# Optimization experiments

Hardware: AMD Instinct MI355X
Metric: run time of the kernel (lower is better)

The kernel has to match this reference:

```python
import jax, jax.numpy as jnp
import numpy as np

B, P, ENC = 64, 196, 2048
A = H = E = 512
V = 30000
L = 30  # max caption length; T = L-1 decode steps


def setup_inputs() -> dict:
    key = jax.random.key(0)
    ks = jax.random.split(key, 24)
    s = 0.02
    lengths = jax.random.randint(ks[1], (B, 1), 2, L + 1)
    lengths = lengths.at[0, 0].set(L)  # ensure max length present
    return {
        "encoder_out": jax.random.normal(ks[0], (B, P, ENC), dtype=jnp.float32),
        "enc_att_w": jax.random.normal(ks[2], (A, ENC), jnp.float32) * s,
        "enc_att_b": jnp.zeros((A,), jnp.float32),
        "dec_att_w": jax.random.normal(ks[3], (A, H), jnp.float32) * s,
        "dec_att_b": jnp.zeros((A,), jnp.float32),
        "full_att_w": jax.random.normal(ks[4], (1, A), jnp.float32) * s,
        "full_att_b": jnp.zeros((1,), jnp.float32),
        "embed": jax.random.uniform(ks[5], (V, E), jnp.float32, -0.1, 0.1),
        "W_ih": jax.random.normal(ks[6], (4 * H, E + ENC), jnp.float32) * s,
        "W_hh": jax.random.normal(ks[7], (4 * H, H), jnp.float32) * s,
        "b_ih": jnp.zeros((4 * H,), jnp.float32),
        "b_hh": jnp.zeros((4 * H,), jnp.float32),
        "init_h_w": jax.random.normal(ks[8], (H, ENC), jnp.float32) * s,
        "init_h_b": jnp.zeros((H,), jnp.float32),
        "init_c_w": jax.random.normal(ks[9], (H, ENC), jnp.float32) * s,
        "init_c_b": jnp.zeros((H,), jnp.float32),
        "f_beta_w": jax.random.normal(ks[10], (ENC, H), jnp.float32) * s,
        "f_beta_b": jnp.zeros((ENC,), jnp.float32),
        "fc_w": jax.random.uniform(ks[11], (V, H), jnp.float32, -0.1, 0.1),
        "fc_b": jnp.zeros((V,), jnp.float32),
        "encoded_captions": jax.random.randint(ks[12], (B, L), 0, V),
        "caption_lengths": lengths,
    }


def reference(encoder_out, enc_att_w, enc_att_b, dec_att_w, dec_att_b, full_att_w,
              full_att_b, embed, W_ih, W_hh, b_ih, b_hh, init_h_w, init_h_b,
              init_c_w, init_c_b, f_beta_w, f_beta_b, fc_w, fc_b,
              encoded_captions, caption_lengths):
    # sort by caption length descending (as in the torch module)
    lengths = caption_lengths[:, 0]
    sort_ind = jnp.argsort(-lengths)
    lengths = lengths[sort_ind]
    enc = encoder_out[sort_ind]               # [B,P,ENC]
    caps = encoded_captions[sort_ind]         # [B,L]
    embeds = embed[caps]                      # [B,L,E]

    mean_enc = enc.mean(axis=1)
    h0 = mean_enc @ init_h_w.T + init_h_b     # [B,H]
    c0 = mean_enc @ init_c_w.T + init_c_b
    dec_len = lengths - 1
    T = caps.shape[1] - 1

    att1 = enc @ enc_att_w.T + enc_att_b      # [B,P,A] (precompute, invariant over t)

    def step(carry, emb_t):
        h, c = carry
        att2 = h @ dec_att_w.T + dec_att_b                                    # [B,A]
        e = jnp.squeeze(jax.nn.relu(att1 + att2[:, None, :]) @ full_att_w.T + full_att_b, -1)  # [B,P]
        alpha = jax.nn.softmax(e, axis=1)
        awe = jnp.einsum('bp,bpd->bd', alpha, enc)                            # [B,ENC]
        gate = jax.nn.sigmoid(h @ f_beta_w.T + f_beta_b)
        awe = gate * awe
        x = jnp.concatenate([emb_t, awe], axis=1)                             # [B,E+ENC]
        gates = x @ W_ih.T + b_ih + h @ W_hh.T + b_hh                         # [B,4H]
        i, f, g, o = jnp.split(gates, 4, axis=1)
        c_new = jax.nn.sigmoid(f) * c + jax.nn.sigmoid(i) * jnp.tanh(g)
        h_new = jax.nn.sigmoid(o) * jnp.tanh(c_new)
        preds = h_new @ fc_w.T + fc_b  # dropout in eval mode = identity
        return (h_new, c_new), (preds, alpha)

    _, (preds, alphas) = jax.lax.scan(step, (h0, c0), jnp.swapaxes(embeds[:, :T], 0, 1))
    preds = jnp.swapaxes(preds, 0, 1)   # [B,T,V]
    alphas = jnp.swapaxes(alphas, 0, 1)  # [B,T,P]
    mask = (jnp.arange(T)[None, :] < dec_len[:, None]).astype(preds.dtype)
    preds = preds * mask[:, :, None]
    alphas = alphas * mask[:, :, None]
    return preds, caps, dec_len, alphas, sort_ind
```

## Files before the change

### kernel.cpp

```cpp
#include <hip/hip_runtime.h>
#include <hip/hip_bf16.h>
#include <cstdint>

#define Bq 64
#define Pq 196
#define ENCq 2048
#define Aq 512
#define Hq 512
#define Vq 30000
#define Lq 30
#define Tq 29

typedef __bf16 bf16x8 __attribute__((ext_vector_type(8)));
typedef float f32x4 __attribute__((ext_vector_type(4)));
typedef __hip_bfloat16 bf16_t;

__device__ __forceinline__ float sigmoidf_(float x){ return 1.0f/(1.0f+expf(-x)); }

__global__ void sort_kernel(const int* __restrict__ cap_len, const int* __restrict__ caps,
                            int* __restrict__ sort_ind_i, int* __restrict__ dec_len_i,
                            int* __restrict__ caps_sorted,
                            float* __restrict__ out_caps, float* __restrict__ out_declen,
                            float* __restrict__ out_sortind)
{
    __shared__ int len[Bq];
    __shared__ int sidx[Bq];
    int i = threadIdx.x;
    len[i] = cap_len[i];
    __syncthreads();
    int li = len[i];
    int rank = 0;
    for (int j = 0; j < Bq; j++){
        int lj = len[j];
        rank += (lj > li) || (lj == li && j < i);
    }
    sidx[rank] = i;
    __syncthreads();
    int src = sidx[i];
    sort_ind_i[i] = src;
    int dl = len[src] - 1;
    dec_len_i[i] = dl;
    out_declen[i] = (float)dl;
    out_sortind[i] = (float)src;
    for (int tt = 0; tt < Lq; tt++){
        int cv = caps[src*Lq + tt];
        caps_sorted[i*Lq + tt] = cv;
        out_caps[i*Lq + tt] = (float)cv;
    }
}

__global__ void cvt_bf16(bf16_t* __restrict__ dst, const float* __restrict__ src, int n)
{
    int i = blockIdx.x*256 + threadIdx.x;
    if (i < n) dst[i] = __float2bfloat16(src[i]);
}

__global__ void pack_rowcat_bf16(bf16_t* __restrict__ dst, const float* __restrict__ a, int na,
                                 const float* __restrict__ b, int nb)
{
    int i = blockIdx.x*256 + threadIdx.x;
    if (i < na) dst[i] = __float2bfloat16(a[i]);
    else if (i < na + nb) dst[i] = __float2bfloat16(b[i - na]);
}

__global__ void pack_rowcat_f32(float* __restrict__ dst, const float* __restrict__ a, int na,
                                const float* __restrict__ b, int nb)
{
    int i = blockIdx.x*256 + threadIdx.x;
    if (i < na) dst[i] = a[i];
    else if (i < na + nb) dst[i] = b[i - na];
}

__global__ void pack_wcatg2(bf16_t* __restrict__ dst, const float* __restrict__ wih,
                            const float* __restrict__ whh)
{
    int i = blockIdx.x*256 + threadIdx.x;
    if (i >= 2048*2560) return;
    int rp = i / 2560, c = i % 2560;
    int g = rp & 3, j = rp >> 2;
    int r = g*512 + j;
    float v = (c < 2048) ? wih[(size_t)r*2560 + 512 + c] : whh[(size_t)r*512 + (c - 2048)];
    dst[i] = __float2bfloat16(v);
}

__global__ void pack_wembg(bf16_t* __restrict__ dst, const float* __restrict__ wih)
{
    int i = blockIdx.x*256 + threadIdx.x;
    if (i >= 2048*512) return;
    int rp = i >> 9, c = i & 511;
    int g = rp & 3, j = rp >> 2;
    int r = g*512 + j;
    dst[i] = __float2bfloat16(wih[(size_t)r*2560 + c]);
}

__global__ void biasg_perm_kernel(float* __restrict__ dst, const float* __restrict__ bi,
                                  const float* __restrict__ bh)
{
    int i = blockIdx.x*256 + threadIdx.x;
    if (i >= 2048) return;
    int g = i & 3, j = i >> 2;
    int r = g*512 + j;
    dst[i] = bi[r] + bh[r];
}

__global__ void gather_emb(const float* __restrict__ embed, const int* __restrict__ caps_sorted,
                           bf16_t* __restrict__ embA)
{
    int m = blockIdx.x;
    int t = m >> 6, b = m & 63;
    int cap = caps_sorted[b*Lq + t];
    const float* er = embed + (size_t)cap*512;
    bf16_t* dr = embA + (size_t)m*512;
    for (int j = threadIdx.x; j < 512; j += 256) dr[j] = __float2bfloat16(er[j]);
}

__global__ __launch_bounds__(256)
void gather_cvt_mean(const float* __restrict__ enc, const int* __restrict__ sort_ind,
                     bf16_t* __restrict__ enc_bf, bf16_t* __restrict__ mean_bf)
{
    int b = blockIdx.x;
    int d = blockIdx.y*256 + threadIdx.x;
    int src = sort_ind[b];
    const float* col = enc + (size_t)src * Pq * ENCq + d;
    bf16_t* dst = enc_bf + (size_t)b * Pq * ENCq + d;
    float s = 0.f;
    for (int p = 0; p < Pq; p++){
        float v = col[(size_t)p*ENCq];
        s += v;
        dst[(size_t)p*ENCq] = __float2bfloat16(v);
    }
    mean_bf[(size_t)b*ENCq + d] = __float2bfloat16(s * (1.0f/196.0f));
}

__global__ __launch_bounds__(256)
void hc0_ksplit(const bf16_t* __restrict__ A, const bf16_t* __restrict__ W,
                const float* __restrict__ bias,
                bf16_t* __restrict__ h0, float* __restrict__ c_state)
{
    __shared__ float red[2][64][64];
    const int lane = threadIdx.x & 63;
    const int wave = threadIdx.x >> 6;
    const int mr = lane & 15;
    const int quad = lane >> 4;
    const int n0 = blockIdx.x * 64;
    const int kw = 2048 >> 2;
    const int kbeg = wave * kw;

    const bf16_t* ap[4];
    const bf16_t* bp[4];
    #pragma unroll
    for (int i = 0; i < 4; i++){
        ap[i] = A + (size_t)(i*16 + mr)*2048 + quad*8;
        bp[i] = W + (size_t)(n0 + i*16 + mr)*2048 + quad*8;
    }
    f32x4 zero = {0.f,0.f,0.f,0.f};
    f32x4 acc[4][4];
    #pragma unroll
    for (int i = 0; i < 4; i++)
        #pragma unroll
        for (int j = 0; j < 4; j++) acc[i][j] = zero;

    for (int k = kbeg; k < kbeg + kw; k += 32){
        bf16x8 a[4], b[4];
        #pragma unroll
        for (int mt = 0; mt < 4; mt++) a[mt] = *(const bf16x8*)(ap[mt] + k);
        #pragma unroll
        for (int nt = 0; nt < 4; nt++) b[nt] = *(const bf16x8*)(bp[nt] + k);
        #pragma unroll
        for (int mt = 0; mt < 4; mt++)
            #pragma unroll
            for (int nt = 0; nt < 4; nt++)
                acc[mt][nt] = __builtin_amdgcn_mfma_f32_16x16x32_bf16(a[mt], b[nt], acc[mt][nt], 0, 0, 0);
    }

    if (wave >= 2){
        #pragma unroll
        for (int mt = 0; mt < 4; mt++)
            #pragma unroll
            for (int nt = 0; nt < 4; nt++)
                #pragma unroll
                for (int r = 0; r < 4; r++)
                    red[wave-2][mt*16 + quad*4 + r][nt*16 + mr] = acc[mt][nt][r];
    }
    __syncthreads();
    if (wave < 2){
        #pragma unroll
        for (int mt = 0; mt < 4; mt++)
            #pragma unroll
            for (int nt = 0; nt < 4; nt++)
                #pragma unroll
                for (int r = 0; r < 4; r++)
                    acc[mt][nt][r] += red[wave][mt*16 + quad*4 + r][nt*16 + mr];
    }
    __syncthreads();
    if (wave == 1){
        #pragma unroll
        for (int mt = 0; mt < 4; mt++)
            #pragma unroll
            for (int nt = 0; nt < 4; nt++)
                #pragma unroll
                for (int r = 0; r < 4; r++)
                    red[0][mt*16 + quad*4 + r][nt*16 + mr] = acc[mt][nt][r];
    }
    __syncthreads();
    if (wave == 0){
        #pragma unroll
        for (int mt = 0; mt < 4; mt++){
            #pragma unroll
            for (int nt = 0; nt < 4; nt++){
                int n = n0 + nt*16 + mr;
                float bv = bias[n];
                #pragma unroll
                for (int r = 0; r < 4; r++){
                    int m = mt*16 + quad*4 + r;
                    float v = acc[mt][nt][r] + red[0][m][nt*16 + mr] + bv;
                    if (n < Hq) h0[(size_t)m*Hq + n] = __float2bfloat16(v);
                    else        c_state[(size_t)m*Hq + (n - Hq)] = v;
                }
            }
        }
    }
}

__global__ __launch_bounds__(256)
void att1_gemm(const bf16_t* __restrict__ A, const bf16_t* __restrict__ W,
               const float* __restrict__ bias, bf16_t* __restrict__ C)
{
    const int lane = threadIdx.x & 63;
    const int wave = threadIdx.x >> 6;
    const int mr = lane & 15;
    const int quad = lane >> 4;
    const int m0 = blockIdx.x * 64;
    const int n0 = (blockIdx.y * 4 + wave) * 64;

    const bf16_t* ap[4];
    const bf16_t* bp[4];
    #pragma unroll
    for (int i = 0; i < 4; i++){
        ap[i] = A + (size_t)(m0 + i*16 + mr)*ENCq + quad*8;
        bp[i] = W + (size_t)(n0 + i*16 + mr)*ENCq + quad*8;
    }
    f32x4 zero = {0.f,0.f,0.f,0.f};
    f32x4 acc[4][4];
    #pragma unroll
    for (int i = 0; i < 4; i++)
        #pragma unroll
        for (int j = 0; j < 4; j++) acc[i][j] = zero;

    for (int k = 0; k < ENCq; k += 32){
        bf16x8 a[4], b[4];
        #pragma unroll
        for (int mt = 0; mt < 4; mt++) a[mt] = *(const bf16x8*)(ap[mt] + k);
        #pragma unroll
        for (int nt = 0; nt < 4; nt++) b[nt] = *(const bf16x8*)(bp[nt] + k);
        #pragma unroll
        for (int mt = 0; mt < 4; mt++)
            #pragma unroll
            for (int nt = 0; nt < 4; nt++)
                acc[mt][nt] = __builtin_amdgcn_mfma_f32_16x16x32_bf16(a[mt], b[nt], acc[mt][nt], 0, 0, 0);
    }
    #pragma unroll
    for (int mt = 0; mt < 4; mt++){
        #pragma unroll
        for (int nt = 0; nt < 4; nt++){
            int n = n0 + nt*16 + mr;
            float bv = bias[n];
            #pragma unroll
            for (int r = 0; r < 4; r++){
                int m = m0 + mt*16 + quad*4 + r;
                C[(size_t)m*Aq + n] = __float2bfloat16(acc[mt][nt][r] + bv);
            }
        }
    }
}

__global__ __launch_bounds__(256)
void embg_gemm(const bf16_t* __restrict__ A, const bf16_t* __restrict__ W,
               float* __restrict__ C)
{
    const int lane = threadIdx.x & 63;
    const int wave = threadIdx.x >> 6;
    const int mr = lane & 15;
    const int quad = lane >> 4;
    const int m0 = blockIdx.x * 64;
    const int n0 = (blockIdx.y * 4 + wave) * 64;

    const bf16_t* ap[4];
    const bf16_t* bp[4];
    #pragma unroll
    for (int i = 0; i < 4; i++){
        ap[i] = A + (size_t)(m0 + i*16 + mr)*512 + quad*8;
        bp[i] = W + (size_t)(n0 + i*16 + mr)*512 + quad*8;
    }
    f32x4 zero = {0.f,0.f,0.f,0.f};
    f32x4 acc[4][4];
    #pragma unroll
    for (int i = 0; i < 4; i++)
        #pragma unroll
        for (int j = 0; j < 4; j++) acc[i][j] = zero;

    #pragma unroll
    for (int kk = 0; kk < 16; kk++){
        bf16x8 a[4], b[4];
        #pragma unroll
        for (int mt = 0; mt < 4; mt++) a[mt] = *(const bf16x8*)(ap[mt] + kk*32);
        #pragma unroll
        for (int nt = 0; nt < 4; nt++) b[nt] = *(const bf16x8*)(bp[nt] + kk*32);
        #pragma unroll
        for (int mt = 0; mt < 4; mt++)
            #pragma unroll
            for (int nt = 0; nt < 4; nt++)
                acc[mt][nt] = __builtin_amdgcn_mfma_f32_16x16x32_bf16(a[mt], b[nt], acc[mt][nt], 0, 0, 0);
    }
    #pragma unroll
    for (int mt = 0; mt < 4; mt++){
        #pragma unroll
        for (int nt = 0; nt < 4; nt++){
            int n = n0 + nt*16 + mr;
            #pragma unroll
            for (int r = 0; r < 4; r++){
                int m = m0 + mt*16 + quad*4 + r;
                C[(size_t)m*2048 + n] = acc[mt][nt][r];
            }
        }
    }
}

__global__ __launch_bounds__(256)
void attg_gemm(const bf16_t* __restrict__ h, const bf16_t* __restrict__ W,
               const float* __restrict__ bias, float* __restrict__ C)
{
    __shared__ __bf16 hs[64][520];
    {
        int r = threadIdx.x >> 2;
        int c0 = (threadIdx.x & 3) * 128;
        const bf16_t* src = h + (size_t)r*512 + c0;
        #pragma unroll
        for (int i = 0; i < 16; i++)
            *(bf16x8*)&hs[r][c0 + i*8] = *(const bf16x8*)(src + i*8);
    }
    __syncthreads();

    const int lane = threadIdx.x & 63;
    const int wave = threadIdx.x >> 6;
    const int mr = lane & 15;
    const int quad = lane >> 4;
    const int n0 = (blockIdx.x * 4 + wave) * 16;

    const bf16_t* bp = W + (size_t)(n0 + mr)*512 + quad*8;
    f32x4 zero = {0.f,0.f,0.f,0.f};
    f32x4 acc[4] = {zero, zero, zero, zero};

    #pragma unroll
    for (int kk = 0; kk < 16; kk++){
        bf16x8 b = *(const bf16x8*)(bp + kk*32);
        bf16x8 a[4];
        #pragma unroll
        for (int mt = 0; mt < 4; mt++)
            a[mt] = *(const bf16x8*)&hs[mt*16 + mr][kk*32 + quad*8];
        #pragma unroll
        for (int mt = 0; mt < 4; mt++)
            acc[mt] = __builtin_amdgcn_mfma_f32_16x16x32_bf16(a[mt], b, acc[mt], 0, 0, 0);
    }

    float bv = bias[n0 + mr];
    #pragma unroll
    for (int mt = 0; mt < 4; mt++){
        #pragma unroll
        for (int r = 0; r < 4; r++){
            int m = mt*16 + quad*4 + r;
            C[(size_t)m*2560 + n0 + mr] = acc[mt][r] + bv;
        }
    }
}

__global__ __launch_bounds__(256)
void gates_lstm2(const bf16_t* __restrict__ A, const bf16_t* __restrict__ W,
                 const float* __restrict__ bias, const float* __restrict__ gE,
                 float* __restrict__ c_state, bf16_t* __restrict__ h_next)
{
    __shared__ float red4[2][64][17];
    const int lane = threadIdx.x & 63;
    const int wid  = threadIdx.x >> 6;
    const int mr = lane & 15;
    const int quad = lane >> 4;
    const int n0 = blockIdx.x * 16;
    const int kbeg = wid * 640;

    const bf16_t* ap[4];
    #pragma unroll
    for (int i = 0; i < 4; i++) ap[i] = A + (size_t)(i*16 + mr)*2560 + quad*8;
    const bf16_t* bp = W + (size_t)(n0 + mr)*2560 + quad*8;

    f32x4 zero = {0.f,0.f,0.f,0.f};
    f32x4 acc[4] = {zero, zero, zero, zero};
    for (int k = kbeg; k < kbeg + 640; k += 32){
        bf16x8 bfr = *(const bf16x8*)(bp + k);
        bf16x8 a[4];
        #pragma unroll
        for (int mt = 0; mt < 4; mt++) a[mt] = *(const bf16x8*)(ap[mt] + k);
        #pragma unroll
        for (int mt = 0; mt < 4; mt++)
            acc[mt] = __builtin_amdgcn_mfma_f32_16x16x32_bf16(a[mt], bfr, acc[mt], 0, 0, 0);
    }
    if (wid >= 2){
        #pragma unroll
        for (int mt = 0; mt < 4; mt++)
            #pragma unroll
            for (int r = 0; r < 4; r++)
                red4[wid-2][mt*16 + quad*4 + r][mr] = acc[mt][r];
    }
    __syncthreads();
    if (wid < 2){
        #pragma unroll
        for (int mt = 0; mt < 4; mt++)
            #pragma unroll
            for (int r = 0; r < 4; r++)
                acc[mt][r] += red4[wid][mt*16 + quad*4 + r][mr];
    }
    __syncthreads();
    if (wid == 1){
        #pragma unroll
        for (int mt = 0; mt < 4; mt++)
            #pragma unroll
            for (int r = 0; r < 4; r++)
                red4[0][mt*16 + quad*4 + r][mr] = acc[mt][r];
    }
    __syncthreads();
    if (wid == 0){
        float bv = bias[n0 + mr];
        #pragma unroll
        for (int mt = 0; mt < 4; mt++){
            #pragma unroll
            for (int r = 0; r < 4; r++){
                int m = mt*16 + quad*4 + r;
                float ge = gE[(size_t)m*2048 + n0 + mr];
                red4[0][m][mr] = acc[mt][r] + red4[0][m][mr] + bv + ge;
            }
        }
    }
    __syncthreads();
    {
        int m = threadIdx.x & 63, jl = threadIdx.x >> 6;
        int j = blockIdx.x*4 + jl;
        float gi = sigmoidf_(red4[0][m][4*jl + 0]);
        float gf = sigmoidf_(red4[0][m][4*jl + 1]);
        float gv = tanhf(red4[0][m][4*jl + 2]);
        float go = sigmoidf_(red4[0][m][4*jl + 3]);
        float cc = c_state[m*512 + j];
        float cn = gf*cc + gi*gv;
        float hn = go * tanhf(cn);
        c_state[m*512 + j] = cn;
        h_next[m*512 + j] = __float2bfloat16(hn);
    }
}

__global__ __launch_bounds__(256)
void preds_batched(const bf16_t* __restrict__ Ah, const bf16_t* __restrict__ W,
                   const float* __restrict__ bias, float* __restrict__ C,
                   const int* __restrict__ dec_len)
{
    const int lane = threadIdx.x & 63;
    const int wave = threadIdx.x >> 6;
    const int mr = lane & 15;
    const int quad = lane >> 4;
    const int m0 = blockIdx.x * 256 + wave * 64;
    const int n0 = blockIdx.y * 64;

    const bf16_t* ap[4];
    const bf16_t* bp[4];
    #pragma unroll
    for (int i = 0; i < 4; i++){
        int row = m0 + i*16 + mr; if (row > 1855) row = 1855;
        ap[i] = Ah + (size_t)row*512 + quad*8;
        int n = n0 + i*16 + mr;   if (n > Vq-1) n = Vq-1;
        bp[i] = W + (size_t)n*512 + quad*8;
    }
    f32x4 zero = {0.f,0.f,0.f,0.f};
    f32x4 acc[4][4];
    #pragma unroll
    for (int i = 0; i < 4; i++)
        #pragma unroll
        for (int j = 0; j < 4; j++) acc[i][j] = zero;

    #pragma unroll
    for (int kk = 0; kk < 16; kk++){
        bf16x8 a[4], b[4];
        #pragma unroll
        for (int mt = 0; mt < 4; mt++) a[mt] = *(const bf16x8*)(ap[mt] + kk*32);
        #pragma unroll
        for (int nt = 0; nt < 4; nt++) b[nt] = *(const bf16x8*)(bp[nt] + kk*32);
        #pragma unroll
        for (int mt = 0; mt < 4; mt++)
            #pragma unroll
            for (int nt = 0; nt < 4; nt++)
                acc[mt][nt] = __builtin_amdgcn_mfma_f32_16x16x32_bf16(b[nt], a[mt], acc[mt][nt], 0, 0, 0);
    }

    #pragma unroll
    for (int mt = 0; mt < 4; mt++){
        int m = m0 + mt*16 + mr;
        if (m >= 1856) continue;
        int tt = m >> 6, b = m & 63;
        bool msk = (tt >= dec_len[b]);
        float* crow = C + (size_t)b*(Tq*Vq) + (size_t)tt*Vq;
        #pragma unroll
        for (int nt = 0; nt < 4; nt++){
            int n = n0 + nt*16 + quad*4;
            if (n < Vq){
                float4 bv = *(const float4*)(bias + n);
                f32x4 v = acc[mt][nt];
                float4 o;
                o.x = msk ? 0.f : (v[0] + bv.x);
                o.y = msk ? 0.f : (v[1] + bv.y);
                o.z = msk ? 0.f : (v[2] + bv.z);
                o.w = msk ? 0.f : (v[3] + bv.w);
                *(float4*)(crow + n) = o;
            }
        }
    }
}

__global__ __launch_bounds__(256)
void attn_kernel(const bf16_t* __restrict__ att1,
                 const float* __restrict__ att2gate,
                 const float* __restrict__ faw, const float* __restrict__ fab,
                 const int* __restrict__ dec_len,
                 float* __restrict__ alpha_ws,
                 float* __restrict__ alphas_out, int t)
{
    __shared__ float es[Pq];
    __shared__ float red[8];
    int b = blockIdx.x;
    int tid = threadIdx.x;
    int wid = tid >> 6, lane = tid & 63;

    float a2r[8], fwr[8];
    {
        const float4* a2p = (const float4*)(att2gate + (size_t)b*2560);
        const float4* fwp = (const float4*)faw;
        float4 u0 = a2p[lane*2], u1 = a2p[lane*2+1];
        float4 w0 = fwp[lane*2], w1 = fwp[lane*2+1];
        a2r[0]=u0.x; a2r[1]=u0.y; a2r[2]=u0.z; a2r[3]=u0.w;
        a2r[4]=u1.x; a2r[5]=u1.y; a2r[6]=u1.z; a2r[7]=u1.w;
        fwr[0]=w0.x; fwr[1]=w0.y; fwr[2]=w0.z; fwr[3]=w0.w;
        fwr[4]=w1.x; fwr[5]=w1.y; fwr[6]=w1.z; fwr[7]=w1.w;
    }
    float fb = fab[0];
    const bf16_t* a1b = att1 + (size_t)b * Pq * Aq + lane*8;
    for (int p = wid; p < Pq; p += 4){
        bf16x8 rv = *(const bf16x8*)(a1b + (size_t)p * Aq);
        float s = 0.f;
        #pragma unroll
        for (int i = 0; i < 8; i++){
            float v = (float)rv[i] + a2r[i];
            v = v > 0.f ? v : 0.f;
            s += v * fwr[i];
        }
        #pragma unroll
        for (int off = 32; off; off >>= 1) s += __shfl_xor(s, off);
        if (lane == 0) es[p] = s + fb;
    }
    __syncthreads();
    float v = (tid < Pq) ? es[tid] : -3.4e38f;
    float m = v;
    #pragma unroll
    for (int off = 32; off; off >>= 1) m = fmaxf(m, __shfl_xor(m, off));
    if ((tid & 63) == 0) red[tid >> 6] = m;
    __syncthreads();
    float bm = fmaxf(fmaxf(red[0], red[1]), fmaxf(red[2], red[3]));
    float ex = (tid < Pq) ? expf(v - bm) : 0.f;
    float s = ex;
    #pragma unroll
    for (int off = 32; off; off >>= 1) s += __shfl_xor(s, off);
    if ((tid & 63) == 0) red[4 + (tid >> 6)] = s;
    __syncthreads();
    float bs = red[4] + red[5] + red[6] + red[7];
    if (tid < Pq){
        float al = ex / bs;
        alpha_ws[b*Pq + tid] = al;
        float mask = (t < dec_len[b]) ? 1.f : 0.f;
        alphas_out[((size_t)b*Tq + t)*Pq + tid] = al * mask;
    }
}

__global__ __launch_bounds__(256)
void awe_xcat2(const bf16_t* __restrict__ enc_bf,
               const float* __restrict__ att2gate,
               const float* __restrict__ alpha_ws,
               const bf16_t* __restrict__ h_prev,
               bf16_t* __restrict__ xcat2)
{
    int b = blockIdx.x, y = blockIdx.y, tid = threadIdx.x;
    __shared__ float als[Pq];
    if (tid < Pq) als[tid] = alpha_ws[b*Pq + tid];
    __syncthreads();
    int d = y*256 + tid;
    const bf16_t* ebase = enc_bf + (size_t)b * Pq * ENCq + d;
    float s = 0.f;
    #pragma unroll 4
    for (int p = 0; p < Pq; p++) s += als[p] * (float)ebase[(size_t)p*ENCq];
    float g = sigmoidf_(att2gate[(size_t)b*2560 + 512 + d]);
    xcat2[(size_t)b*2560 + d] = __float2bfloat16(g * s);
    if (y == 0){
        for (int j = tid; j < 512; j += 256)
            xcat2[(size_t)b*2560 + 2048 + j] = h_prev[b*512 + j];
    }
}

extern "C" void kernel_launch(void* const* d_in, const int* in_sizes, int n_in,
                              void* d_out, int out_size, void* d_ws, size_t ws_size,
                              hipStream_t stream)
{
    const float* encoder_out = (const float*)d_in[0];
    const float* enc_att_w   = (const float*)d_in[1];
    const float* enc_att_b   = (const float*)d_in[2];
    const float* dec_att_w   = (const float*)d_in[3];
    const float* dec_att_b   = (const float*)d_in[4];
    const float* full_att_w  = (const float*)d_in[5];
    const float* full_att_b  = (const float*)d_in[6];
    const float* embed       = (const float*)d_in[7];
    const float* W_ih        = (const float*)d_in[8];
    const float* W_hh        = (const float*)d_in[9];
    const float* b_ih        = (const float*)d_in[10];
    const float* b_hh        = (const float*)d_in[11];
    const float* init_h_w    = (const float*)d_in[12];
    const float* init_h_b    = (const float*)d_in[13];
    const float* init_c_w    = (const float*)d_in[14];
    const float* init_c_b    = (const float*)d_in[15];
    const float* f_beta_w    = (const float*)d_in[16];
    const float* f_beta_b    = (const float*)d_in[17];
    const float* fc_w        = (const float*)d_in[18];
    const float* fc_b        = (const float*)d_in[19];
    const int*   enc_caps    = (const int*)d_in[20];
    const int*   cap_len     = (const int*)d_in[21];

    float* out_preds   = (float*)d_out;
    float* out_caps    = out_preds + (size_t)Bq*Tq*Vq;
    float* out_declen  = out_caps + Bq*Lq;
    float* out_alphas  = out_declen + Bq;
    float* out_sortind = out_alphas + (size_t)Bq*Tq*Pq;

    char* cur = (char*)d_ws;
    auto alloc = [&](size_t bytes) -> char* {
        char* p = cur;
        cur += (bytes + 255) & ~(size_t)255;
        return p;
    };
    bf16_t* enc_bf    = (bf16_t*)alloc((size_t)12544*2048*2);
    bf16_t* att1_bf   = (bf16_t*)alloc((size_t)12544*512*2);
    bf16_t* fcw_bf    = (bf16_t*)alloc((size_t)30000*512*2);
    bf16_t* wcatg_bf  = (bf16_t*)alloc((size_t)2048*2560*2);
    bf16_t* wembg_bf  = (bf16_t*)alloc((size_t)2048*512*2);
    bf16_t* embA_bf   = (bf16_t*)alloc((size_t)1856*512*2);
    float*  gatesE    = (float*)alloc((size_t)1856*2048*4);
    bf16_t* whc_bf    = (bf16_t*)alloc((size_t)1024*2048*2);
    bf16_t* wcat2_bf  = (bf16_t*)alloc((size_t)2560*512*2);
    bf16_t* encattw_bf= (bf16_t*)alloc((size_t)512*2048*2);
    bf16_t* meanenc_bf= (bf16_t*)alloc((size_t)64*2048*2);
    bf16_t* h_hist    = (bf16_t*)alloc((size_t)30*64*512*2);
    bf16_t* xcat2_bf  = (bf16_t*)alloc((size_t)64*2560*2);
    float* c_state   = (float*)alloc((size_t)64*512*4);
    float* att2gate  = (float*)alloc((size_t)64*2560*4);
    float* bias_hc   = (float*)alloc(1024*4);
    float* bias2     = (float*)alloc(2560*4);
    float* bias_g    = (float*)alloc(2048*4);
    float* alpha_ws  = (float*)alloc((size_t)64*196*4);
    int* caps_sorted = (int*)alloc(Bq*Lq*4);
    int* sort_ind_i  = (int*)alloc(64*4);
    int* dec_len_i   = (int*)alloc(64*4);

    sort_kernel<<<1, 64, 0, stream>>>(cap_len, enc_caps, sort_ind_i, dec_len_i,
                                      caps_sorted, out_caps, out_declen, out_sortind);

    cvt_bf16<<<(1048576+255)/256, 256, 0, stream>>>(encattw_bf, enc_att_w, 1048576);
    cvt_bf16<<<(15360000+255)/256, 256, 0, stream>>>(fcw_bf, fc_w, 15360000);
    pack_rowcat_bf16<<<(2097152+255)/256, 256, 0, stream>>>(whc_bf, init_h_w, 1048576, init_c_w, 1048576);
    pack_rowcat_bf16<<<(1310720+255)/256, 256, 0, stream>>>(wcat2_bf, dec_att_w, 262144, f_beta_w, 1048576);
    pack_wcatg2<<<(2048*2560+255)/256, 256, 0, stream>>>(wcatg_bf, W_ih, W_hh);
    pack_wembg<<<(2048*512+255)/256, 256, 0, stream>>>(wembg_bf, W_ih);
    pack_rowcat_f32<<<(1024+255)/256, 256, 0, stream>>>(bias_hc, init_h_b, 512, init_c_b, 512);
    pack_rowcat_f32<<<(2560+255)/256, 256, 0, stream>>>(bias2, dec_att_b, 512, f_beta_b, 2048);
    biasg_perm_kernel<<<8, 256, 0, stream>>>(bias_g, b_ih, b_hh);

    gather_emb<<<1856, 256, 0, stream>>>(embed, caps_sorted, embA_bf);
    embg_gemm<<<dim3(29,8), 256, 0, stream>>>(embA_bf, wembg_bf, gatesE);

    gather_cvt_mean<<<dim3(64,8), 256, 0, stream>>>(encoder_out, sort_ind_i, enc_bf, meanenc_bf);

    hc0_ksplit<<<16, 256, 0, stream>>>(meanenc_bf, whc_bf, bias_hc, h_hist, c_state);

    att1_gemm<<<dim3(196,2), 256, 0, stream>>>(enc_bf, encattw_bf, enc_att_b, att1_bf);

    for (int t = 0; t < Tq; t++){
        const bf16_t* h_prev = h_hist + (size_t)t*Bq*Hq;
        bf16_t* h_next = h_hist + (size_t)(t+1)*Bq*Hq;

        attg_gemm<<<40, 256, 0, stream>>>(h_prev, wcat2_bf, bias2, att2gate);

        attn_kernel<<<64, 256, 0, stream>>>(att1_bf, att2gate, full_att_w, full_att_b,
                                            dec_len_i, alpha_ws, out_alphas, t);

        awe_xcat2<<<dim3(64,8), 256, 0, stream>>>(enc_bf, att2gate, alpha_ws, h_prev, xcat2_bf);

        gates_lstm2<<<128, 256, 0, stream>>>(xcat2_bf, wcatg_bf, bias_g,
                                             gatesE + (size_t)t*64*2048, c_state, h_next);
    }

    preds_batched<<<dim3(8,469), 256, 0, stream>>>(h_hist + (size_t)Bq*Hq, fcw_bf, fc_b,
                                                   out_preds, dec_len_i);
}
```

Before: 3.005 ms.

## Fuse per-step attention projections, softmax and gated context into one kernel

```diff
diff --git a/kernel.cpp b/kernel.cpp
--- a/kernel.cpp
+++ b/kernel.cpp
@@ -12,6 +12,7 @@
 #define Tq 29
 
 typedef __bf16 bf16x8 __attribute__((ext_vector_type(8)));
+typedef __bf16 bf16x4 __attribute__((ext_vector_type(4)));
 typedef float f32x4 __attribute__((ext_vector_type(4)));
 typedef __hip_bfloat16 bf16_t;
 
@@ -326,52 +327,130 @@
     }
 }
 
-__global__ __launch_bounds__(256)
-void attg_gemm(const bf16_t* __restrict__ h, const bf16_t* __restrict__ W,
-               const float* __restrict__ bias, float* __restrict__ C)
-{
-    __shared__ __bf16 hs[64][520];
+__global__ __launch_bounds__(512)
+void attn_fused(const bf16_t* __restrict__ att1, const bf16_t* __restrict__ wcat2,
+                const float* __restrict__ bias2, const float* __restrict__ faw,
+                const float* __restrict__ fab, const int* __restrict__ dec_len,
+                const bf16_t* __restrict__ enc_bf, const bf16_t* __restrict__ h_prev,
+                float* __restrict__ alphas_out, bf16_t* __restrict__ xcat2, int t)
+{
+    __shared__ float hls[512];
+    __shared__ float a2s[512];
+    __shared__ float es[Pq];
+    __shared__ float als[Pq];
+    __shared__ float red[16];
+    const int b = blockIdx.x;
+    const int tid = threadIdx.x;
+    const int wid = tid >> 6, lane = tid & 63;
+    const bf16_t* hp = h_prev + (size_t)b*512;
+
+    if (tid < 64){
+        bf16x8 hv = ((const bf16x8*)hp)[tid];
+        #pragma unroll
+        for (int i = 0; i < 8; i++) hls[tid*8 + i] = (float)hv[i];
+    }
+    __syncthreads();
+
     {
-        int r = threadIdx.x >> 2;
-        int c0 = (threadIdx.x & 3) * 128;
-        const bf16_t* src = h + (size_t)r*512 + c0;
-        #pragma unroll
-        for (int i = 0; i < 16; i++)
-            *(bf16x8*)&hs[r][c0 + i*8] = *(const bf16x8*)(src + i*8);
-    }
-    __syncthreads();
-
-    const int lane = threadIdx.x & 63;
-    const int wave = threadIdx.x >> 6;
-    const int mr = lane & 15;
-    const int quad = lane >> 4;
-    const int n0 = (blockIdx.x * 4 + wave) * 16;
-
-    const bf16_t* bp = W + (size_t)(n0 + mr)*512 + quad*8;
-    f32x4 zero = {0.f,0.f,0.f,0.f};
-    f32x4 acc[4] = {zero, zero, zero, zero};
-
-    #pragma unroll
-    for (int kk = 0; kk < 16; kk++){
-        bf16x8 b = *(const bf16x8*)(bp + kk*32);
-        bf16x8 a[4];
-        #pragma unroll
-        for (int mt = 0; mt < 4; mt++)
-            a[mt] = *(const bf16x8*)&hs[mt*16 + mr][kk*32 + quad*8];
-        #pragma unroll
-        for (int mt = 0; mt < 4; mt++)
-            acc[mt] = __builtin_amdgcn_mfma_f32_16x16x32_bf16(a[mt], b, acc[mt], 0, 0, 0);
-    }
-
-    float bv = bias[n0 + mr];
-    #pragma unroll
-    for (int mt = 0; mt < 4; mt++){
+        const bf16_t* wr = wcat2 + (size_t)tid*512;
+        float s = 0.f;
+        for (int k = 0; k < 512; k += 8){
+            bf16x8 w = *(const bf16x8*)(wr + k);
+            float4 h0 = *(const float4*)&hls[k];
+            float4 h1 = *(const float4*)&hls[k+4];
+            s += h0.x*(float)w[0] + h0.y*(float)w[1] + h0.z*(float)w[2] + h0.w*(float)w[3]
+               + h1.x*(float)w[4] + h1.y*(float)w[5] + h1.z*(float)w[6] + h1.w*(float)w[7];
+        }
+        a2s[tid] = s + bias2[tid];
+    }
+    __syncthreads();
+
+    {
+        float a2r[8], fwr[8];
+        const float4* fwp = (const float4*)faw;
+        float4 w0 = fwp[lane*2], w1 = fwp[lane*2+1];
+        fwr[0]=w0.x; fwr[1]=w0.y; fwr[2]=w0.z; fwr[3]=w0.w;
+        fwr[4]=w1.x; fwr[5]=w1.y; fwr[6]=w1.z; fwr[7]=w1.w;
+        #pragma unroll
+        for (int i = 0; i < 8; i++) a2r[i] = a2s[lane*8 + i];
+        float fb = fab[0];
+        const bf16_t* a1b = att1 + (size_t)b * Pq * Aq + lane*8;
+        for (int p = wid; p < Pq; p += 8){
+            bf16x8 rv = *(const bf16x8*)(a1b + (size_t)p * Aq);
+            float s = 0.f;
+            #pragma unroll
+            for (int i = 0; i < 8; i++){
+                float v = (float)rv[i] + a2r[i];
+                v = v > 0.f ? v : 0.f;
+                s += v * fwr[i];
+            }
+            #pragma unroll
+            for (int off = 32; off; off >>= 1) s += __shfl_xor(s, off);
+            if (lane == 0) es[p] = s + fb;
+        }
+    }
+    __syncthreads();
+
+    {
+        float v = (tid < Pq) ? es[tid] : -3.4e38f;
+        float m = v;
+        #pragma unroll
+        for (int off = 32; off; off >>= 1) m = fmaxf(m, __shfl_xor(m, off));
+        if (lane == 0) red[wid] = m;
+        __syncthreads();
+        float bm = red[0];
+        #pragma unroll
+        for (int w = 1; w < 8; w++) bm = fmaxf(bm, red[w]);
+        float ex = (tid < Pq) ? expf(v - bm) : 0.f;
+        float s = ex;
+        #pragma unroll
+        for (int off = 32; off; off >>= 1) s += __shfl_xor(s, off);
+        if (lane == 0) red[8 + wid] = s;
+        __syncthreads();
+        float bs = red[8];
+        #pragma unroll
+        for (int w = 1; w < 8; w++) bs += red[8 + w];
+        if (tid < Pq){
+            float al = ex / bs;
+            als[tid] = al;
+            float mask = (t < dec_len[b]) ? 1.f : 0.f;
+            alphas_out[((size_t)b*Tq + t)*Pq + tid] = al * mask;
+        }
+    }
+    __syncthreads();
+
+    {
+        const int d0 = tid * 4;
+        const bf16_t* wr = wcat2 + (size_t)(512 + d0)*512;
+        f32x4 gs = {0.f,0.f,0.f,0.f};
+        for (int k = 0; k < 512; k += 8){
+            float4 h0 = *(const float4*)&hls[k];
+            float4 h1 = *(const float4*)&hls[k+4];
+            #pragma unroll
+            for (int r = 0; r < 4; r++){
+                bf16x8 w = *(const bf16x8*)(wr + (size_t)r*512 + k);
+                gs[r] += h0.x*(float)w[0] + h0.y*(float)w[1] + h0.z*(float)w[2] + h0.w*(float)w[3]
+                       + h1.x*(float)w[4] + h1.y*(float)w[5] + h1.z*(float)w[6] + h1.w*(float)w[7];
+            }
+        }
+        const bf16_t* eb = enc_bf + (size_t)b * Pq * ENCq + d0;
+        f32x4 sa = {0.f,0.f,0.f,0.f};
+        for (int p = 0; p < Pq; p++){
+            bf16x4 ev = *(const bf16x4*)(eb + (size_t)p*ENCq);
+            float al = als[p];
+            sa[0] += al*(float)ev[0];
+            sa[1] += al*(float)ev[1];
+            sa[2] += al*(float)ev[2];
+            sa[3] += al*(float)ev[3];
+        }
+        bf16_t* xo = xcat2 + (size_t)b*2560 + d0;
         #pragma unroll
         for (int r = 0; r < 4; r++){
-            int m = mt*16 + quad*4 + r;
-            C[(size_t)m*2560 + n0 + mr] = acc[mt][r] + bv;
-        }
-    }
+            float g = sigmoidf_(gs[r] + bias2[512 + d0 + r]);
+            xo[r] = __float2bfloat16(g * sa[r]);
+        }
+    }
+    xcat2[(size_t)b*2560 + 2048 + tid] = hp[tid];
 }
 
 __global__ __launch_bounds__(256)
@@ -456,155 +535,78 @@
 }
 
 __global__ __launch_bounds__(256)
-void preds_batched(const bf16_t* __restrict__ Ah, const bf16_t* __restrict__ W,
-                   const float* __restrict__ bias, float* __restrict__ C,
-                   const int* __restrict__ dec_len)
-{
-    const int lane = threadIdx.x & 63;
-    const int wave = threadIdx.x >> 6;
+void preds_batched2(const bf16_t* __restrict__ Ah, const bf16_t* __restrict__ W,
+                    const float* __restrict__ bias, float* __restrict__ C,
+                    const int* __restrict__ dec_len)
+{
+    __shared__ __bf16 Ws[64][520];
+    const int tid = threadIdx.x;
+    const int lane = tid & 63;
+    const int wave = tid >> 6;
     const int mr = lane & 15;
     const int quad = lane >> 4;
-    const int m0 = blockIdx.x * 256 + wave * 64;
-    const int n0 = blockIdx.y * 64;
-
-    const bf16_t* ap[4];
-    const bf16_t* bp[4];
-    #pragma unroll
-    for (int i = 0; i < 4; i++){
-        int row = m0 + i*16 + mr; if (row > 1855) row = 1855;
-        ap[i] = Ah + (size_t)row*512 + quad*8;
-        int n = n0 + i*16 + mr;   if (n > Vq-1) n = Vq-1;
-        bp[i] = W + (size_t)n*512 + quad*8;
-    }
-    f32x4 zero = {0.f,0.f,0.f,0.f};
-    f32x4 acc[4][4];
-    #pragma unroll
-    for (int i = 0; i < 4; i++)
-        #pragma unroll
-        for (int j = 0; j < 4; j++) acc[i][j] = zero;
-
-    #pragma unroll
-    for (int kk = 0; kk < 16; kk++){
-        bf16x8 a[4], b[4];
-        #pragma unroll
-        for (int mt = 0; mt < 4; mt++) a[mt] = *(const bf16x8*)(ap[mt] + kk*32);
-        #pragma unroll
-        for (int nt = 0; nt < 4; nt++) b[nt] = *(const bf16x8*)(bp[nt] + kk*32);
-        #pragma unroll
-        for (int mt = 0; mt < 4; mt++)
-            #pragma unroll
-            for (int nt = 0; nt < 4; nt++)
-                acc[mt][nt] = __builtin_amdgcn_mfma_f32_16x16x32_bf16(b[nt], a[mt], acc[mt][nt], 0, 0, 0);
-    }
-
-    #pragma unroll
-    for (int mt = 0; mt < 4; mt++){
-        int m = m0 + mt*16 + mr;
-        if (m >= 1856) continue;
-        int tt = m >> 6, b = m & 63;
-        bool msk = (tt >= dec_len[b]);
-        float* crow = C + (size_t)b*(Tq*Vq) + (size_t)tt*Vq;
-        #pragma unroll
-        for (int nt = 0; nt < 4; nt++){
-            int n = n0 + nt*16 + quad*4;
-            if (n < Vq){
-                float4 bv = *(const float4*)(bias + n);
-                f32x4 v = acc[mt][nt];
-                float4 o;
-                o.x = msk ? 0.f : (v[0] + bv.x);
-                o.y = msk ? 0.f : (v[1] + bv.y);
-                o.z = msk ? 0.f : (v[2] + bv.z);
-                o.w = msk ? 0.f : (v[3] + bv.w);
-                *(float4*)(crow + n) = o;
+    const int n0 = blockIdx.x * 64;
+
+    {
+        int r = tid >> 2;
+        int c0 = (tid & 3) * 128;
+        int row = n0 + r; if (row > Vq-1) row = Vq-1;
+        const bf16_t* src = W + (size_t)row*512 + c0;
+        #pragma unroll
+        for (int i = 0; i < 16; i++)
+            *(bf16x8*)&Ws[r][c0 + i*8] = *(const bf16x8*)(src + i*8);
+    }
+    __syncthreads();
+
+    for (int mi = wave; mi < 29; mi += 4){
+        const int m0 = mi * 64;
+        const bf16_t* ap[4];
+        #pragma unroll
+        for (int i = 0; i < 4; i++)
+            ap[i] = Ah + (size_t)(m0 + i*16 + mr)*512 + quad*8;
+
+        f32x4 zero = {0.f,0.f,0.f,0.f};
+        f32x4 acc[4][4];
+        #pragma unroll
+        for (int i = 0; i < 4; i++)
+            #pragma unroll
+            for (int j = 0; j < 4; j++) acc[i][j] = zero;
+
+        #pragma unroll
+        for (int kk = 0; kk < 16; kk++){
+            bf16x8 a[4], bw[4];
+            #pragma unroll
+            for (int mt = 0; mt < 4; mt++) a[mt] = *(const bf16x8*)(ap[mt] + kk*32);
+            #pragma unroll
+            for (int nt = 0; nt < 4; nt++) bw[nt] = *(const bf16x8*)&Ws[nt*16 + mr][kk*32 + quad*8];
+            #pragma unroll
+            for (int mt = 0; mt < 4; mt++)
+                #pragma unroll
+                for (int nt = 0; nt < 4; nt++)
+                    acc[mt][nt] = __builtin_amdgcn_mfma_f32_16x16x32_bf16(bw[nt], a[mt], acc[mt][nt], 0, 0, 0);
+        }
+
+        #pragma unroll
+        for (int mt = 0; mt < 4; mt++){
+            int m = m0 + mt*16 + mr;
+            int tt = m >> 6, bb = m & 63;
+            bool msk = (tt >= dec_len[bb]);
+            float* crow = C + (size_t)bb*(Tq*Vq) + (size_t)tt*Vq;
+            #pragma unroll
+            for (int nt = 0; nt < 4; nt++){
+                int n = n0 + nt*16 + quad*4;
+                if (n < Vq){
+                    float4 bv = *(const float4*)(bias + n);
+                    f32x4 v = acc[mt][nt];
+                    float4 o;
+                    o.x = msk ? 0.f : (v[0] + bv.x);
+                    o.y = msk ? 0.f : (v[1] + bv.y);
+                    o.z = msk ? 0.f : (v[2] + bv.z);
+                    o.w = msk ? 0.f : (v[3] + bv.w);
+                    *(float4*)(crow + n) = o;
+                }
             }
         }
-    }
-}
-
-__global__ __launch_bounds__(256)
-void attn_kernel(const bf16_t* __restrict__ att1,
-                 const float* __restrict__ att2gate,
-                 const float* __restrict__ faw, const float* __restrict__ fab,
-                 const int* __restrict__ dec_len,
-                 float* __restrict__ alpha_ws,
-                 float* __restrict__ alphas_out, int t)
-{
-    __shared__ float es[Pq];
-    __shared__ float red[8];
-    int b = blockIdx.x;
-    int tid = threadIdx.x;
-    int wid = tid >> 6, lane = tid & 63;
-
-    float a2r[8], fwr[8];
-    {
-        const float4* a2p = (const float4*)(att2gate + (size_t)b*2560);
-        const float4* fwp = (const float4*)faw;
-        float4 u0 = a2p[lane*2], u1 = a2p[lane*2+1];
-        float4 w0 = fwp[lane*2], w1 = fwp[lane*2+1];
-        a2r[0]=u0.x; a2r[1]=u0.y; a2r[2]=u0.z; a2r[3]=u0.w;
-        a2r[4]=u1.x; a2r[5]=u1.y; a2r[6]=u1.z; a2r[7]=u1.w;
-        fwr[0]=w0.x; fwr[1]=w0.y; fwr[2]=w0.z; fwr[3]=w0.w;
-        fwr[4]=w1.x; fwr[5]=w1.y; fwr[6]=w1.z; fwr[7]=w1.w;
-    }
-    float fb = fab[0];
-    const bf16_t* a1b = att1 + (size_t)b * Pq * Aq + lane*8;
-    for (int p = wid; p < Pq; p += 4){
-        bf16x8 rv = *(const bf16x8*)(a1b + (size_t)p * Aq);
-        float s = 0.f;
-        #pragma unroll
-        for (int i = 0; i < 8; i++){
-            float v = (float)rv[i] + a2r[i];
-            v = v > 0.f ? v : 0.f;
-            s += v * fwr[i];
-        }
-        #pragma unroll
-        for (int off = 32; off; off >>= 1) s += __shfl_xor(s, off);
-        if (lane == 0) es[p] = s + fb;
-    }
-    __syncthreads();
-    float v = (tid < Pq) ? es[tid] : -3.4e38f;
-    float m = v;
-    #pragma unroll
-    for (int off = 32; off; off >>= 1) m = fmaxf(m, __shfl_xor(m, off));
-    if ((tid & 63) == 0) red[tid >> 6] = m;
-    __syncthreads();
-    float bm = fmaxf(fmaxf(red[0], red[1]), fmaxf(red[2], red[3]));
-    float ex = (tid < Pq) ? expf(v - bm) : 0.f;
-    float s = ex;
-    #pragma unroll
-    for (int off = 32; off; off >>= 1) s += __shfl_xor(s, off);
-    if ((tid & 63) == 0) red[4 + (tid >> 6)] = s;
-    __syncthreads();
-    float bs = red[4] + red[5] + red[6] + red[7];
-    if (tid < Pq){
-        float al = ex / bs;
-        alpha_ws[b*Pq + tid] = al;
-        float mask = (t < dec_len[b]) ? 1.f : 0.f;
-        alphas_out[((size_t)b*Tq + t)*Pq + tid] = al * mask;
-    }
-}
-
-__global__ __launch_bounds__(256)
-void awe_xcat2(const bf16_t* __restrict__ enc_bf,
-               const float* __restrict__ att2gate,
-               const float* __restrict__ alpha_ws,
-               const bf16_t* __restrict__ h_prev,
-               bf16_t* __restrict__ xcat2)
-{
-    int b = blockIdx.x, y = blockIdx.y, tid = threadIdx.x;
-    __shared__ float als[Pq];
-    if (tid < Pq) als[tid] = alpha_ws[b*Pq + tid];
-    __syncthreads();
-    int d = y*256 + tid;
-    const bf16_t* ebase = enc_bf + (size_t)b * Pq * ENCq + d;
-    float s = 0.f;
-    #pragma unroll 4
-    for (int p = 0; p < Pq; p++) s += als[p] * (float)ebase[(size_t)p*ENCq];
-    float g = sigmoidf_(att2gate[(size_t)b*2560 + 512 + d]);
-    xcat2[(size_t)b*2560 + d] = __float2bfloat16(g * s);
-    if (y == 0){
-        for (int j = tid; j < 512; j += 256)
-            xcat2[(size_t)b*2560 + 2048 + j] = h_prev[b*512 + j];
     }
 }
 
@@ -661,11 +663,9 @@
     bf16_t* h_hist    = (bf16_t*)alloc((size_t)30*64*512*2);
     bf16_t* xcat2_bf  = (bf16_t*)alloc((size_t)64*2560*2);
     float* c_state   = (float*)alloc((size_t)64*512*4);
-    float* att2gate  = (float*)alloc((size_t)64*2560*4);
     float* bias_hc   = (float*)alloc(1024*4);
     float* bias2     = (float*)alloc(2560*4);
     float* bias_g    = (float*)alloc(2048*4);
-    float* alpha_ws  = (float*)alloc((size_t)64*196*4);
     int* caps_sorted = (int*)alloc(Bq*Lq*4);
     int* sort_ind_i  = (int*)alloc(64*4);
     int* dec_len_i   = (int*)alloc(64*4);
@@ -696,17 +696,13 @@
         const bf16_t* h_prev = h_hist + (size_t)t*Bq*Hq;
         bf16_t* h_next = h_hist + (size_t)(t+1)*Bq*Hq;
 
-        attg_gemm<<<40, 256, 0, stream>>>(h_prev, wcat2_bf, bias2, att2gate);
-
-        attn_kernel<<<64, 256, 0, stream>>>(att1_bf, att2gate, full_att_w, full_att_b,
-                                            dec_len_i, alpha_ws, out_alphas, t);
-
-        awe_xcat2<<<dim3(64,8), 256, 0, stream>>>(enc_bf, att2gate, alpha_ws, h_prev, xcat2_bf);
+        attn_fused<<<64, 512, 0, stream>>>(att1_bf, wcat2_bf, bias2, full_att_w, full_att_b,
+                                           dec_len_i, enc_bf, h_prev, out_alphas, xcat2_bf, t);
 
         gates_lstm2<<<128, 256, 0, stream>>>(xcat2_bf, wcatg_bf, bias_g,
                                              gatesE + (size_t)t*64*2048, c_state, h_next);
     }
 
-    preds_batched<<<dim3(8,469), 256, 0, stream>>>(h_hist + (size_t)Bq*Hq, fcw_bf, fc_b,
-                                                   out_preds, dec_len_i);
-}
+    preds_batched2<<<469, 256, 0, stream>>>(h_hist + (size_t)Bq*Hq, fcw_bf, fc_b,
+                                            out_preds, dec_len_i);
+}
```

Measured after the change: 4.589 ms. 52.7% more time.

## Fuse attention softmax with weighted encoding and swizzle preds grid per XCD

Applied to the files above, without the earlier changes.

```diff
diff --git a/kernel.cpp b/kernel.cpp
--- a/kernel.cpp
+++ b/kernel.cpp
@@ -374,6 +374,91 @@
     }
 }
 
+__global__ __launch_bounds__(512)
+void awe_attn(const bf16_t* __restrict__ att1, const float* __restrict__ att2gate,
+              const float* __restrict__ faw, const float* __restrict__ fab,
+              const int* __restrict__ dec_len, const bf16_t* __restrict__ enc_bf,
+              const bf16_t* __restrict__ h_prev, float* __restrict__ alphas_out,
+              bf16_t* __restrict__ xcat2, int t)
+{
+    __shared__ float es[Pq];
+    __shared__ float als[Pq];
+    __shared__ float red[16];
+    const int b = blockIdx.x, y = blockIdx.y;
+    const int tid = threadIdx.x;
+    const int wid = tid >> 6, lane = tid & 63;
+
+    {
+        float a2r[8], fwr[8];
+        const float4* a2p = (const float4*)(att2gate + (size_t)b*2560);
+        const float4* fwp = (const float4*)faw;
+        float4 u0 = a2p[lane*2], u1 = a2p[lane*2+1];
+        float4 w0 = fwp[lane*2], w1 = fwp[lane*2+1];
+        a2r[0]=u0.x; a2r[1]=u0.y; a2r[2]=u0.z; a2r[3]=u0.w;
+        a2r[4]=u1.x; a2r[5]=u1.y; a2r[6]=u1.z; a2r[7]=u1.w;
+        fwr[0]=w0.x; fwr[1]=w0.y; fwr[2]=w0.z; fwr[3]=w0.w;
+        fwr[4]=w1.x; fwr[5]=w1.y; fwr[6]=w1.z; fwr[7]=w1.w;
+        float fb = fab[0];
+        const bf16_t* a1b = att1 + (size_t)b * Pq * Aq + lane*8;
+        for (int p = wid; p < Pq; p += 8){
+            bf16x8 rv = *(const bf16x8*)(a1b + (size_t)p * Aq);
+            float s = 0.f;
+            #pragma unroll
+            for (int i = 0; i < 8; i++){
+                float v = (float)rv[i] + a2r[i];
+                v = v > 0.f ? v : 0.f;
+                s += v * fwr[i];
+            }
+            #pragma unroll
+            for (int off = 32; off; off >>= 1) s += __shfl_xor(s, off);
+            if (lane == 0) es[p] = s + fb;
+        }
+    }
+    __syncthreads();
+
+    {
+        float v = (tid < Pq) ? es[tid] : -3.4e38f;
+        float m = v;
+        #pragma unroll
+        for (int off = 32; off; off >>= 1) m = fmaxf(m, __shfl_xor(m, off));
+        if (lane == 0) red[wid] = m;
+        __syncthreads();
+        float bm = red[0];
+        #pragma unroll
+        for (int w = 1; w < 8; w++) bm = fmaxf(bm, red[w]);
+        float ex = (tid < Pq) ? expf(v - bm) : 0.f;
+        float s = ex;
+        #pragma unroll
+        for (int off = 32; off; off >>= 1) s += __shfl_xor(s, off);
+        if (lane == 0) red[8 + wid] = s;
+        __syncthreads();
+        float bs = red[8];
+        #pragma unroll
+        for (int w = 1; w < 8; w++) bs += red[8 + w];
+        if (tid < Pq){
+            float al = ex / bs;
+            als[tid] = al;
+            if (y == 0){
+                float mask = (t < dec_len[b]) ? 1.f : 0.f;
+                alphas_out[((size_t)b*Tq + t)*Pq + tid] = al * mask;
+            }
+        }
+    }
+    __syncthreads();
+
+    {
+        int d = y*512 + tid;
+        const bf16_t* ebase = enc_bf + (size_t)b * Pq * ENCq + d;
+        float s = 0.f;
+        #pragma unroll 4
+        for (int p = 0; p < Pq; p++) s += als[p] * (float)ebase[(size_t)p*ENCq];
+        float g = sigmoidf_(att2gate[(size_t)b*2560 + 512 + d]);
+        xcat2[(size_t)b*2560 + d] = __float2bfloat16(g * s);
+    }
+    if (y == 0)
+        xcat2[(size_t)b*2560 + 2048 + tid] = h_prev[(size_t)b*512 + tid];
+}
+
 __global__ __launch_bounds__(256)
 void gates_lstm2(const bf16_t* __restrict__ A, const bf16_t* __restrict__ W,
                  const float* __restrict__ bias, const float* __restrict__ gE,
@@ -460,12 +545,18 @@
                    const float* __restrict__ bias, float* __restrict__ C,
                    const int* __restrict__ dec_len)
 {
+    const int id = blockIdx.x;
+    const int q = id & 7;
+    const int r = id >> 3;
+    const int vy = q*59 + (r >> 3);
+    const int vx = r & 7;
+
     const int lane = threadIdx.x & 63;
     const int wave = threadIdx.x >> 6;
     const int mr = lane & 15;
     const int quad = lane >> 4;
-    const int m0 = blockIdx.x * 256 + wave * 64;
-    const int n0 = blockIdx.y * 64;
+    const int m0 = vx * 256 + wave * 64;
+    const int n0 = vy * 64;
 
     const bf16_t* ap[4];
     const bf16_t* bp[4];
@@ -518,93 +609,6 @@
                 *(float4*)(crow + n) = o;
             }
         }
-    }
-}
-
-__global__ __launch_bounds__(256)
-void attn_kernel(const bf16_t* __restrict__ att1,
-                 const float* __restrict__ att2gate,
-                 const float* __restrict__ faw, const float* __restrict__ fab,
-                 const int* __restrict__ dec_len,
-                 float* __restrict__ alpha_ws,
-                 float* __restrict__ alphas_out, int t)
-{
-    __shared__ float es[Pq];
-    __shared__ float red[8];
-    int b = blockIdx.x;
-    int tid = threadIdx.x;
-    int wid = tid >> 6, lane = tid & 63;
-
-    float a2r[8], fwr[8];
-    {
-        const float4* a2p = (const float4*)(att2gate + (size_t)b*2560);
-        const float4* fwp = (const float4*)faw;
-        float4 u0 = a2p[lane*2], u1 = a2p[lane*2+1];
-        float4 w0 = fwp[lane*2], w1 = fwp[lane*2+1];
-        a2r[0]=u0.x; a2r[1]=u0.y; a2r[2]=u0.z; a2r[3]=u0.w;
-        a2r[4]=u1.x; a2r[5]=u1.y; a2r[6]=u1.z; a2r[7]=u1.w;
-        fwr[0]=w0.x; fwr[1]=w0.y; fwr[2]=w0.z; fwr[3]=w0.w;
-        fwr[4]=w1.x; fwr[5]=w1.y; fwr[6]=w1.z; fwr[7]=w1.w;
-    }
-    float fb = fab[0];
-    const bf16_t* a1b = att1 + (size_t)b * Pq * Aq + lane*8;
-    for (int p = wid; p < Pq; p += 4){
-        bf16x8 rv = *(const bf16x8*)(a1b + (size_t)p * Aq);
-        float s = 0.f;
-        #pragma unroll
-        for (int i = 0; i < 8; i++){
-            float v = (float)rv[i] + a2r[i];
-            v = v > 0.f ? v : 0.f;
-            s += v * fwr[i];
-        }
-        #pragma unroll
-        for (int off = 32; off; off >>= 1) s += __shfl_xor(s, off);
-        if (lane == 0) es[p] = s + fb;
-    }
-    __syncthreads();
-    float v = (tid < Pq) ? es[tid] : -3.4e38f;
-    float m = v;
-    #pragma unroll
-    for (int off = 32; off; off >>= 1) m = fmaxf(m, __shfl_xor(m, off));
-    if ((tid & 63) == 0) red[tid >> 6] = m;
-    __syncthreads();
-    float bm = fmaxf(fmaxf(red[0], red[1]), fmaxf(red[2], red[3]));
-    float ex = (tid < Pq) ? expf(v - bm) : 0.f;
-    float s = ex;
-    #pragma unroll
-    for (int off = 32; off; off >>= 1) s += __shfl_xor(s, off);
-    if ((tid & 63) == 0) red[4 + (tid >> 6)] = s;
-    __syncthreads();
-    float bs = red[4] + red[5] + red[6] + red[7];
-    if (tid < Pq){
-        float al = ex / bs;
-        alpha_ws[b*Pq + tid] = al;
-        float mask = (t < dec_len[b]) ? 1.f : 0.f;
-        alphas_out[((size_t)b*Tq + t)*Pq + tid] = al * mask;
-    }
-}
-
-__global__ __launch_bounds__(256)
-void awe_xcat2(const bf16_t* __restrict__ enc_bf,
-               const float* __restrict__ att2gate,
-               const float* __restrict__ alpha_ws,
-               const bf16_t* __restrict__ h_prev,
-               bf16_t* __restrict__ xcat2)
-{
-    int b = blockIdx.x, y = blockIdx.y, tid = threadIdx.x;
-    __shared__ float als[Pq];
-    if (tid < Pq) als[tid] = alpha_ws[b*Pq + tid];
-    __syncthreads();
-    int d = y*256 + tid;
-    const bf16_t* ebase = enc_bf + (size_t)b * Pq * ENCq + d;
-    float s = 0.f;
-    #pragma unroll 4
-    for (int p = 0; p < Pq; p++) s += als[p] * (float)ebase[(size_t)p*ENCq];
-    float g = sigmoidf_(att2gate[(size_t)b*2560 + 512 + d]);
-    xcat2[(size_t)b*2560 + d] = __float2bfloat16(g * s);
-    if (y == 0){
-        for (int j = tid; j < 512; j += 256)
-            xcat2[(size_t)b*2560 + 2048 + j] = h_prev[b*512 + j];
     }
 }
 
@@ -665,7 +669,6 @@
     float* bias_hc   = (float*)alloc(1024*4);
     float* bias2     = (float*)alloc(2560*4);
     float* bias_g    = (float*)alloc(2048*4);
-    float* alpha_ws  = (float*)alloc((size_t)64*196*4);
     int* caps_sorted = (int*)alloc(Bq*Lq*4);
     int* sort_ind_i  = (int*)alloc(64*4);
     int* dec_len_i   = (int*)alloc(64*4);
@@ -698,15 +701,13 @@
 
         attg_gemm<<<40, 256, 0, stream>>>(h_prev, wcat2_bf, bias2, att2gate);
 
-        attn_kernel<<<64, 256, 0, stream>>>(att1_bf, att2gate, full_att_w, full_att_b,
-                                            dec_len_i, alpha_ws, out_alphas, t);
-
-        awe_xcat2<<<dim3(64,8), 256, 0, stream>>>(enc_bf, att2gate, alpha_ws, h_prev, xcat2_bf);
+        awe_attn<<<dim3(64,4), 512, 0, stream>>>(att1_bf, att2gate, full_att_w, full_att_b,
+                                                 dec_len_i, enc_bf, h_prev, out_alphas, xcat2_bf, t);
 
         gates_lstm2<<<128, 256, 0, stream>>>(xcat2_bf, wcatg_bf, bias_g,
                                              gatesE + (size_t)t*64*2048, c_state, h_next);
     }
 
-    preds_batched<<<dim3(8,469), 256, 0, stream>>>(h_hist + (size_t)Bq*Hq, fcw_bf, fc_b,
-                                                   out_preds, dec_len_i);
-}
+    preds_batched<<<3776, 256, 0, stream>>>(h_hist + (size_t)Bq*Hq, fcw_bf, fc_b,
+                                            out_preds, dec_len_i);
+}
```

Result: faster. 2.565 ms (-14.7%).
